# Kernel tuning notes

Hardware: AMD Instinct MI355X
Metric: run time of the kernel (lower is better)

## Reference

```python
import jax, jax.numpy as jnp
import numpy as np

N_NODES = 50000
N_EDGES = 600000
N_GRAPHS = 500


def gcn_conv(x, src, dst, W, b, n_nodes):
    # PyG GCNConv: add self-loops, symmetric normalization D^-1/2 (A+I) D^-1/2, then XW + b
    h = x @ W  # [N, F_out]
    loop = jnp.arange(n_nodes)
    s = jnp.concatenate([src, loop])
    d = jnp.concatenate([dst, loop])
    deg = jax.ops.segment_sum(jnp.ones_like(d, dtype=h.dtype), d, num_segments=n_nodes)
    dinv = jnp.where(deg > 0, jax.lax.rsqrt(jnp.maximum(deg, 1.0)), 0.0)
    norm = dinv[s] * dinv[d]  # [E+N]
    msg = h[s] * norm[:, None]  # gather + scale
    out = jax.ops.segment_sum(msg, d, num_segments=n_nodes)  # scatter-add
    return out + b


def setup_inputs() -> dict:
    key = jax.random.key(0)
    ks = jax.random.split(key, 12)
    F_in, H, Hf, D_out = 128, 128, 64, 1
    x = jax.random.normal(ks[0], (N_NODES, F_in), dtype=jnp.float32)
    edge_index = jax.random.randint(ks[1], (2, N_EDGES), 0, N_NODES, dtype=jnp.int64)
    batch = jnp.sort(jax.random.randint(ks[2], (N_NODES,), 0, N_GRAPHS, dtype=jnp.int64))
    def glorot(k, shape):
        lim = np.sqrt(6.0 / (shape[0] + shape[1]))
        return jax.random.uniform(k, shape, jnp.float32, -lim, lim)
    return {
        "x": x, "edge_index": edge_index, "batch": batch,
        "W1": glorot(ks[3], (F_in, H)), "b1": jnp.zeros((H,), jnp.float32),
        "W2": glorot(ks[4], (H, H)), "b2": jnp.zeros((H,), jnp.float32),
        "W3": glorot(ks[5], (H, H)), "b3": jnp.zeros((H,), jnp.float32),
        "Wf1": glorot(ks[6], (H, Hf)), "bf1": jnp.zeros((Hf,), jnp.float32),
        "Wf2": glorot(ks[7], (Hf, D_out)), "bf2": jnp.zeros((D_out,), jnp.float32),
    }


def reference(x, edge_index, batch, W1, b1, W2, b2, W3, b3, Wf1, bf1, Wf2, bf2):
    src, dst = edge_index[0], edge_index[1]
    n = x.shape[0]
    h = jax.nn.relu(gcn_conv(x, src, dst, W1, b1, n))
    h = jax.nn.relu(gcn_conv(h, src, dst, W2, b2, n))
    h = jax.nn.relu(gcn_conv(h, src, dst, W3, b3, n))
    # global_mean_pool: segment mean over graphs
    sums = jax.ops.segment_sum(h, batch, num_segments=N_GRAPHS)
    cnts = jax.ops.segment_sum(jnp.ones((n,), h.dtype), batch, num_segments=N_GRAPHS)
    hg = sums / jnp.maximum(cnts, 1.0)[:, None]  # [G, 128]
    h = jax.nn.relu(hg @ Wf1 + bf1)
    return h @ Wf2 + bf2
```

## Files before the change

kernel.cpp:

```cpp
#include <hip/hip_runtime.h>

#define N_NODES 50000
#define N_EDGES 600000
#define N_GRAPHS 500
#define F 128

typedef short bf16x8 __attribute__((ext_vector_type(8)));
typedef float f32x4 __attribute__((ext_vector_type(4)));
union U4H8 { uint4 u; bf16x8 h; };

__device__ inline unsigned pk_bf16(float a, float b) {
    unsigned ua = __float_as_uint(a), ub = __float_as_uint(b);
    ua = (ua + 0x7fffu + ((ua >> 16) & 1u)) >> 16;
    ub = (ub + 0x7fffu + ((ub >> 16) & 1u)) >> 16;
    return ua | (ub << 16);
}
__device__ inline float bf16_rnd(float x) {
    unsigned u = __float_as_uint(x);
    u = (u + 0x7fffu + ((u >> 16) & 1u)) & 0xffff0000u;
    return __uint_as_float(u);
}
#define BF_LO(u) __uint_as_float((u) << 16)
#define BF_HI(u) __uint_as_float((u) & 0xffff0000u)

__global__ __launch_bounds__(256) void k_cvt(const float* __restrict__ x,
                                             unsigned short* __restrict__ xb, int n8) {
    int idx = blockIdx.x * 256 + threadIdx.x;
    if (idx < n8) {
        const float4* xr = (const float4*)(x + (size_t)idx * 8);
        float4 a = xr[0], b = xr[1];
        uint4 o;
        o.x = pk_bf16(a.x, a.y); o.y = pk_bf16(a.z, a.w);
        o.z = pk_bf16(b.x, b.y); o.w = pk_bf16(b.z, b.w);
        ((uint4*)xb)[idx] = o;
    }
}

__global__ __launch_bounds__(256) void k_hist(const int* __restrict__ dst, int* __restrict__ cnt, int ne) {
    int e = blockIdx.x * 256 + threadIdx.x;
    if (e < ne) atomicAdd(&cnt[dst[e]], 1);
}

__global__ __launch_bounds__(256) void k_scan1(const int* __restrict__ cnt, int* __restrict__ row_ptr,
                                               int* __restrict__ blksums, float* __restrict__ dinv, int n) {
    __shared__ int s[256];
    int i = blockIdx.x * 256 + threadIdx.x;
    int v = (i < n) ? cnt[i] : 0;
    if (i < n) dinv[i] = rsqrtf((float)(v + 1));
    s[threadIdx.x] = v;
    __syncthreads();
    for (int off = 1; off < 256; off <<= 1) {
        int t = (threadIdx.x >= off) ? s[threadIdx.x - off] : 0;
        __syncthreads();
        s[threadIdx.x] += t;
        __syncthreads();
    }
    if (i < n) row_ptr[i] = s[threadIdx.x] - v;
    if (threadIdx.x == 255) blksums[blockIdx.x] = s[255];
}

__global__ __launch_bounds__(256) void k_scan2(int* __restrict__ blksums, int nb) {
    __shared__ int s[256];
    int v = (threadIdx.x < nb) ? blksums[threadIdx.x] : 0;
    s[threadIdx.x] = v;
    __syncthreads();
    for (int off = 1; off < 256; off <<= 1) {
        int t = (threadIdx.x >= off) ? s[threadIdx.x - off] : 0;
        __syncthreads();
        s[threadIdx.x] += t;
        __syncthreads();
    }
    if (threadIdx.x < nb) blksums[threadIdx.x] = s[threadIdx.x] - v;
}

__global__ __launch_bounds__(256) void k_scan3(int* __restrict__ row_ptr, const int* __restrict__ blksums,
                                               int n, int ne) {
    int i = blockIdx.x * 256 + threadIdx.x;
    if (i < n) row_ptr[i] += blksums[blockIdx.x];
    if (i == 0) row_ptr[n] = ne;
}

__global__ __launch_bounds__(256) void k_fill(const int* __restrict__ src, const int* __restrict__ dst,
                                              const int* __restrict__ row_ptr, int* __restrict__ cnt,
                                              const float* __restrict__ dinv,
                                              int2* __restrict__ esw, int ne) {
    int e = blockIdx.x * 256 + threadIdx.x;
    if (e < ne) {
        int d = dst[e];
        int s = src[e];
        int pos = row_ptr[d] + atomicSub(&cnt[d], 1) - 1;
        esw[pos] = make_int2(s, __float_as_int(dinv[s]));
    }
}

__global__ __launch_bounds__(256) void k_prepW(const float* __restrict__ W1, const float* __restrict__ W2,
                                               const float* __restrict__ W3,
                                               uint4* __restrict__ Whi, uint4* __restrict__ Wlo) {
    int idx = blockIdx.x * 256 + threadIdx.x;
    int layer = idx >> 11;
    const float* W = (layer == 0) ? W1 : (layer == 1) ? W2 : W3;
    int t = idx & 2047;
    int lane = t & 63, sc = t >> 6;
    int s = sc >> 3, c = sc & 7;
    int q = lane >> 4, m = lane & 15;
    int k0 = 32 * s + 8 * q, n0 = 16 * c + m;
    float w[8], h[8];
    #pragma unroll
    for (int j = 0; j < 8; ++j) {
        w[j] = W[(k0 + j) * F + n0];
        h[j] = bf16_rnd(w[j]);
    }
    uint4 uh, ul;
    uh.x = pk_bf16(h[0], h[1]); uh.y = pk_bf16(h[2], h[3]);
    uh.z = pk_bf16(h[4], h[5]); uh.w = pk_bf16(h[6], h[7]);
    ul.x = pk_bf16(w[0] - h[0], w[1] - h[1]); ul.y = pk_bf16(w[2] - h[2], w[3] - h[3]);
    ul.z = pk_bf16(w[4] - h[4], w[5] - h[5]); ul.w = pk_bf16(w[6] - h[6], w[7] - h[7]);
    Whi[idx] = uh;
    Wlo[idx] = ul;
}

#define TN 32
#define GP 132
__global__ __launch_bounds__(256) void k_fused(const int* __restrict__ row_ptr,
                                               const int2* __restrict__ esw,
                                               const float* __restrict__ dinv,
                                               const unsigned short* __restrict__ Hin,
                                               const uint4* __restrict__ Whi,
                                               const uint4* __restrict__ Wlo,
                                               const float* __restrict__ bias,
                                               unsigned short* __restrict__ Hout, int n) {
    __shared__ float G[TN * GP];
    int tid = threadIdx.x;
    int d0 = blockIdx.x * TN;
    int grp = tid >> 4, sub = tid & 15;

    #pragma unroll
    for (int i = 0; i < 2; ++i) {
        int nl = 2 * grp + i;
        int node = d0 + nl;
        float4 accL = make_float4(0.f, 0.f, 0.f, 0.f);
        float4 accH = make_float4(0.f, 0.f, 0.f, 0.f);
        if (node < n) {
            int beg = row_ptr[node], end = row_ptr[node + 1];
            float dd = dinv[node];
            for (int chunk = beg; chunk <= end; chunk += 16) {
                int e = chunk + sub;
                int2 rec;
                if (e < end)       rec = esw[e];
                else if (e == end) rec = make_int2(node, __float_as_int(dd));
                else               rec = make_int2(node, 0);
                uint4 rows[16];
                #pragma unroll
                for (int j = 0; j < 16; ++j) {
                    int sj = __shfl(rec.x, j, 16);
                    rows[j] = ((const uint4*)(Hin + (size_t)sj * F))[sub];
                }
                #pragma unroll
                for (int j = 0; j < 16; ++j) {
                    float wj = __uint_as_float((unsigned)__shfl(rec.y, j, 16)) * dd;
                    accL.x = fmaf(BF_LO(rows[j].x), wj, accL.x);
                    accL.y = fmaf(BF_HI(rows[j].x), wj, accL.y);
                    accL.z = fmaf(BF_LO(rows[j].y), wj, accL.z);
                    accL.w = fmaf(BF_HI(rows[j].y), wj, accL.w);
                    accH.x = fmaf(BF_LO(rows[j].z), wj, accH.x);
                    accH.y = fmaf(BF_HI(rows[j].z), wj, accH.y);
                    accH.z = fmaf(BF_LO(rows[j].w), wj, accH.z);
                    accH.w = fmaf(BF_HI(rows[j].w), wj, accH.w);
                }
            }
        }
        float* gr = &G[nl * GP + 8 * sub];
        ((float4*)gr)[0] = accL;
        ((float4*)gr)[1] = accH;
    }
    __syncthreads();

    int wave = tid >> 6, lane = tid & 63;
    int q = lane >> 4, m = lane & 15;
    int rt = wave & 1;
    int ch = (wave >> 1) * 4;
    int row0 = 16 * rt;
    f32x4 acc[4];
    #pragma unroll
    for (int c = 0; c < 4; ++c) acc[c] = (f32x4){0.f, 0.f, 0.f, 0.f};
    #pragma unroll
    for (int s = 0; s < 4; ++s) {
        const float* gr = &G[(row0 + m) * GP + 32 * s + 8 * q];
        float4 f0 = ((const float4*)gr)[0];
        float4 f1 = ((const float4*)gr)[1];
        float h0 = bf16_rnd(f0.x), h1 = bf16_rnd(f0.y), h2 = bf16_rnd(f0.z), h3 = bf16_rnd(f0.w);
        float h4 = bf16_rnd(f1.x), h5 = bf16_rnd(f1.y), h6 = bf16_rnd(f1.z), h7 = bf16_rnd(f1.w);
        U4H8 ahi, alo;
        ahi.u.x = (__float_as_uint(h0) >> 16) | (__float_as_uint(h1) & 0xffff0000u);
        ahi.u.y = (__float_as_uint(h2) >> 16) | (__float_as_uint(h3) & 0xffff0000u);
        ahi.u.z = (__float_as_uint(h4) >> 16) | (__float_as_uint(h5) & 0xffff0000u);
        ahi.u.w = (__float_as_uint(h6) >> 16) | (__float_as_uint(h7) & 0xffff0000u);
        alo.u.x = pk_bf16(f0.x - h0, f0.y - h1);
        alo.u.y = pk_bf16(f0.z - h2, f0.w - h3);
        alo.u.z = pk_bf16(f1.x - h4, f1.y - h5);
        alo.u.w = pk_bf16(f1.z - h6, f1.w - h7);
        #pragma unroll
        for (int cc = 0; cc < 4; ++cc) {
            int c = ch + cc;
            U4H8 bh, bl;
            bh.u = Whi[(s * 8 + c) * 64 + lane];
            bl.u = Wlo[(s * 8 + c) * 64 + lane];
            acc[cc] = __builtin_amdgcn_mfma_f32_16x16x32_bf16(ahi.h, bh.h, acc[cc], 0, 0, 0);
            acc[cc] = __builtin_amdgcn_mfma_f32_16x16x32_bf16(alo.h, bh.h, acc[cc], 0, 0, 0);
            acc[cc] = __builtin_amdgcn_mfma_f32_16x16x32_bf16(ahi.h, bl.h, acc[cc], 0, 0, 0);
        }
    }
    __syncthreads();

    #pragma unroll
    for (int cc = 0; cc < 4; ++cc) {
        int c = ch + cc;
        float bb = bias[16 * c + m];
        #pragma unroll
        for (int r = 0; r < 4; ++r)
            G[(row0 + 4 * q + r) * GP + 16 * c + m] = fmaxf(acc[cc][r] + bb, 0.f);
    }
    __syncthreads();
    #pragma unroll
    for (int j = 0; j < 2; ++j) {
        int lin = tid + 256 * j;
        int row = lin >> 4, c8 = lin & 15;
        int node = d0 + row;
        if (node < n) {
            const float* gr = &G[row * GP + c8 * 8];
            uint4 o;
            o.x = pk_bf16(gr[0], gr[1]);
            o.y = pk_bf16(gr[2], gr[3]);
            o.z = pk_bf16(gr[4], gr[5]);
            o.w = pk_bf16(gr[6], gr[7]);
            ((uint4*)(Hout + (size_t)node * F))[c8] = o;
        }
    }
}

__global__ __launch_bounds__(256) void k_pool_fc(const unsigned short* __restrict__ Hb,
                                                 const int* __restrict__ batch,
                                                 const float* __restrict__ Wf1,
                                                 const float* __restrict__ bf1,
                                                 const float* __restrict__ Wf2,
                                                 const float* __restrict__ bf2,
                                                 float* __restrict__ out) {
    int g = blockIdx.x;
    int tid = threadIdx.x;
    int lo = 0, hi = N_NODES;
    while (lo < hi) { int mid = (lo + hi) >> 1; if (batch[mid] < g) lo = mid + 1; else hi = mid; }
    int start = lo;
    hi = N_NODES;
    while (lo < hi) { int mid = (lo + hi) >> 1; if (batch[mid] <= g) lo = mid + 1; else hi = mid; }
    int end = lo;

    __shared__ float hs[4][F];
    __shared__ float hg[F];
    int wv = tid >> 6, lane = tid & 63;
    int half = lane >> 5, sub = lane & 31;
    float4 a = make_float4(0.f, 0.f, 0.f, 0.f);
    for (int i = start + wv * 2 + half; i < end; i += 8) {
        uint2 v = ((const uint2*)(Hb + (size_t)i * F))[sub];
        a.x += BF_LO(v.x); a.y += BF_HI(v.x);
        a.z += BF_LO(v.y); a.w += BF_HI(v.y);
    }
    a.x += __shfl_xor(a.x, 32, 64);
    a.y += __shfl_xor(a.y, 32, 64);
    a.z += __shfl_xor(a.z, 32, 64);
    a.w += __shfl_xor(a.w, 32, 64);
    if (half == 0) ((float4*)hs[wv])[sub] = a;
    __syncthreads();
    if (tid < F) {
        float inv = 1.0f / (float)((end - start) > 0 ? (end - start) : 1);
        hg[tid] = (hs[0][tid] + hs[1][tid] + hs[2][tid] + hs[3][tid]) * inv;
    }
    __syncthreads();
    if (tid < 64) {
        float acc = bf1[tid];
        #pragma unroll 4
        for (int f = 0; f < F; ++f) acc = fmaf(hg[f], Wf1[f * 64 + tid], acc);
        float v = fmaxf(acc, 0.f) * Wf2[tid];
        #pragma unroll
        for (int off = 32; off > 0; off >>= 1) v += __shfl_down(v, off, 64);
        if (tid == 0) out[g] = v + bf2[0];
    }
}

extern "C" void kernel_launch(void* const* d_in, const int* in_sizes, int n_in,
                              void* d_out, int out_size, void* d_ws, size_t ws_size,
                              hipStream_t stream) {
    const float* x    = (const float*)d_in[0];
    const int* eidx   = (const int*)d_in[1];
    const int* batch  = (const int*)d_in[2];
    const float* W1   = (const float*)d_in[3];
    const float* b1   = (const float*)d_in[4];
    const float* W2   = (const float*)d_in[5];
    const float* b2   = (const float*)d_in[6];
    const float* W3   = (const float*)d_in[7];
    const float* b3   = (const float*)d_in[8];
    const float* Wf1  = (const float*)d_in[9];
    const float* bf1  = (const float*)d_in[10];
    const float* Wf2  = (const float*)d_in[11];
    const float* bf2  = (const float*)d_in[12];
    float* out = (float*)d_out;

    const int* src = eidx;
    const int* dst = eidx + N_EDGES;

    char* p = (char*)d_ws;
    unsigned short* Xb  = (unsigned short*)p;  p += (size_t)N_NODES * F * 2;
    unsigned short* H1  = (unsigned short*)p;  p += (size_t)N_NODES * F * 2;
    unsigned short* H2  = (unsigned short*)p;  p += (size_t)N_NODES * F * 2;
    unsigned short* H3  = (unsigned short*)p;  p += (size_t)N_NODES * F * 2;
    int2* esw   = (int2*)p;    p += (size_t)N_EDGES * sizeof(int2);
    uint4* Whi  = (uint4*)p;   p += (size_t)3 * 2048 * sizeof(uint4);
    uint4* Wlo  = (uint4*)p;   p += (size_t)3 * 2048 * sizeof(uint4);
    float* dinv = (float*)p;   p += (size_t)N_NODES * sizeof(float);
    int* cnt     = (int*)p;    p += (size_t)N_NODES * sizeof(int);
    int* row_ptr = (int*)p;    p += (size_t)(N_NODES + 1) * sizeof(int);
    int* blksums = (int*)p;    p += 256 * sizeof(int);

    dim3 b256(256);
    int gNodes = (N_NODES + 255) / 256;
    int gEdges = (N_EDGES + 255) / 256;
    int gCvt   = (N_NODES * F / 8 + 255) / 256;
    int gFused = (N_NODES + TN - 1) / TN;

    k_cvt<<<gCvt, b256, 0, stream>>>(x, Xb, N_NODES * F / 8);
    k_prepW<<<24, b256, 0, stream>>>(W1, W2, W3, Whi, Wlo);

    hipMemsetAsync(cnt, 0, (size_t)N_NODES * sizeof(int), stream);
    k_hist<<<gEdges, b256, 0, stream>>>(dst, cnt, N_EDGES);
    k_scan1<<<gNodes, b256, 0, stream>>>(cnt, row_ptr, blksums, dinv, N_NODES);
    k_scan2<<<1, b256, 0, stream>>>(blksums, gNodes);
    k_scan3<<<gNodes, b256, 0, stream>>>(row_ptr, blksums, N_NODES, N_EDGES);
    k_fill<<<gEdges, b256, 0, stream>>>(src, dst, row_ptr, cnt, dinv, esw, N_EDGES);

    k_fused<<<gFused, b256, 0, stream>>>(row_ptr, esw, dinv, Xb, Whi,        Wlo,        b1, H1, N_NODES);
    k_fused<<<gFused, b256, 0, stream>>>(row_ptr, esw, dinv, H1, Whi + 2048, Wlo + 2048, b2, H2, N_NODES);
    k_fused<<<gFused, b256, 0, stream>>>(row_ptr, esw, dinv, H2, Whi + 4096, Wlo + 4096, b3, H3, N_NODES);

    k_pool_fc<<<N_GRAPHS, b256, 0, stream>>>(H3, batch, Wf1, bf1, Wf2, bf2, out);
}
```

Before: 292.0 us.

## Merge prep kernels, prefetch next edge chunk, and add occupancy hint

Folds the bf16 conversion of x, the in-degree histogram and the weight hi/lo split into one launch that dispatches on block index, removing two kernel launches and their gaps. In the fused aggregation kernel, the next chunk's edge records are now loaded before the FMA loop so that their latency overlaps compute, and the shuffles are split into separate batches. It also adds a launch_bounds minimum of 4 blocks per CU, which may cap registers and risk spills given the 16 uint4 row buffer. Padding lanes now gather row 0 instead of the node's own row.

```diff
diff --git a/kernel.cpp b/kernel.cpp
--- a/kernel.cpp
+++ b/kernel.cpp
@@ -23,22 +23,52 @@
 #define BF_LO(u) __uint_as_float((u) << 16)
 #define BF_HI(u) __uint_as_float((u) & 0xffff0000u)
 
-__global__ __launch_bounds__(256) void k_cvt(const float* __restrict__ x,
-                                             unsigned short* __restrict__ xb, int n8) {
-    int idx = blockIdx.x * 256 + threadIdx.x;
-    if (idx < n8) {
-        const float4* xr = (const float4*)(x + (size_t)idx * 8);
-        float4 a = xr[0], b = xr[1];
-        uint4 o;
-        o.x = pk_bf16(a.x, a.y); o.y = pk_bf16(a.z, a.w);
-        o.z = pk_bf16(b.x, b.y); o.w = pk_bf16(b.z, b.w);
-        ((uint4*)xb)[idx] = o;
-    }
-}
-
-__global__ __launch_bounds__(256) void k_hist(const int* __restrict__ dst, int* __restrict__ cnt, int ne) {
-    int e = blockIdx.x * 256 + threadIdx.x;
-    if (e < ne) atomicAdd(&cnt[dst[e]], 1);
+#define G_CVT  3125
+#define G_HIST 2344
+#define G_PREPW 24
+
+__global__ __launch_bounds__(256) void k_prep(const float* __restrict__ x, unsigned short* __restrict__ xb,
+                                              const int* __restrict__ dst, int* __restrict__ cnt,
+                                              const float* __restrict__ W1, const float* __restrict__ W2,
+                                              const float* __restrict__ W3,
+                                              uint4* __restrict__ Whi, uint4* __restrict__ Wlo) {
+    int b = blockIdx.x, tid = threadIdx.x;
+    if (b < G_CVT) {
+        int idx = b * 256 + tid;
+        if (idx < N_NODES * F / 8) {
+            const float4* xr = (const float4*)(x + (size_t)idx * 8);
+            float4 a = xr[0], c = xr[1];
+            uint4 o;
+            o.x = pk_bf16(a.x, a.y); o.y = pk_bf16(a.z, a.w);
+            o.z = pk_bf16(c.x, c.y); o.w = pk_bf16(c.z, c.w);
+            ((uint4*)xb)[idx] = o;
+        }
+    } else if (b < G_CVT + G_HIST) {
+        int e = (b - G_CVT) * 256 + tid;
+        if (e < N_EDGES) atomicAdd(&cnt[dst[e]], 1);
+    } else {
+        int idx = (b - G_CVT - G_HIST) * 256 + tid;
+        int layer = idx >> 11;
+        const float* W = (layer == 0) ? W1 : (layer == 1) ? W2 : W3;
+        int t = idx & 2047;
+        int lane = t & 63, sc = t >> 6;
+        int s = sc >> 3, c = sc & 7;
+        int q = lane >> 4, m = lane & 15;
+        int k0 = 32 * s + 8 * q, n0 = 16 * c + m;
+        float w[8], h[8];
+        #pragma unroll
+        for (int j = 0; j < 8; ++j) {
+            w[j] = W[(k0 + j) * F + n0];
+            h[j] = bf16_rnd(w[j]);
+        }
+        uint4 uh, ul;
+        uh.x = pk_bf16(h[0], h[1]); uh.y = pk_bf16(h[2], h[3]);
+        uh.z = pk_bf16(h[4], h[5]); uh.w = pk_bf16(h[6], h[7]);
+        ul.x = pk_bf16(w[0] - h[0], w[1] - h[1]); ul.y = pk_bf16(w[2] - h[2], w[3] - h[3]);
+        ul.z = pk_bf16(w[4] - h[4], w[5] - h[5]); ul.w = pk_bf16(w[6] - h[6], w[7] - h[7]);
+        Whi[idx] = uh;
+        Wlo[idx] = ul;
+    }
 }
 
 __global__ __launch_bounds__(256) void k_scan1(const int* __restrict__ cnt, int* __restrict__ row_ptr,
@@ -93,42 +123,16 @@
     }
 }
 
-__global__ __launch_bounds__(256) void k_prepW(const float* __restrict__ W1, const float* __restrict__ W2,
-                                               const float* __restrict__ W3,
-                                               uint4* __restrict__ Whi, uint4* __restrict__ Wlo) {
-    int idx = blockIdx.x * 256 + threadIdx.x;
-    int layer = idx >> 11;
-    const float* W = (layer == 0) ? W1 : (layer == 1) ? W2 : W3;
-    int t = idx & 2047;
-    int lane = t & 63, sc = t >> 6;
-    int s = sc >> 3, c = sc & 7;
-    int q = lane >> 4, m = lane & 15;
-    int k0 = 32 * s + 8 * q, n0 = 16 * c + m;
-    float w[8], h[8];
-    #pragma unroll
-    for (int j = 0; j < 8; ++j) {
-        w[j] = W[(k0 + j) * F + n0];
-        h[j] = bf16_rnd(w[j]);
-    }
-    uint4 uh, ul;
-    uh.x = pk_bf16(h[0], h[1]); uh.y = pk_bf16(h[2], h[3]);
-    uh.z = pk_bf16(h[4], h[5]); uh.w = pk_bf16(h[6], h[7]);
-    ul.x = pk_bf16(w[0] - h[0], w[1] - h[1]); ul.y = pk_bf16(w[2] - h[2], w[3] - h[3]);
-    ul.z = pk_bf16(w[4] - h[4], w[5] - h[5]); ul.w = pk_bf16(w[6] - h[6], w[7] - h[7]);
-    Whi[idx] = uh;
-    Wlo[idx] = ul;
-}
-
 #define TN 32
 #define GP 132
-__global__ __launch_bounds__(256) void k_fused(const int* __restrict__ row_ptr,
-                                               const int2* __restrict__ esw,
-                                               const float* __restrict__ dinv,
-                                               const unsigned short* __restrict__ Hin,
-                                               const uint4* __restrict__ Whi,
-                                               const uint4* __restrict__ Wlo,
-                                               const float* __restrict__ bias,
-                                               unsigned short* __restrict__ Hout, int n) {
+__global__ __launch_bounds__(256, 4) void k_fused(const int* __restrict__ row_ptr,
+                                                  const int2* __restrict__ esw,
+                                                  const float* __restrict__ dinv,
+                                                  const unsigned short* __restrict__ Hin,
+                                                  const uint4* __restrict__ Whi,
+                                                  const uint4* __restrict__ Wlo,
+                                                  const float* __restrict__ bias,
+                                                  unsigned short* __restrict__ Hout, int n) {
     __shared__ float G[TN * GP];
     int tid = threadIdx.x;
     int d0 = blockIdx.x * TN;
@@ -143,21 +147,32 @@
         if (node < n) {
             int beg = row_ptr[node], end = row_ptr[node + 1];
             float dd = dinv[node];
-            for (int chunk = beg; chunk <= end; chunk += 16) {
-                int e = chunk + sub;
-                int2 rec;
-                if (e < end)       rec = esw[e];
-                else if (e == end) rec = make_int2(node, __float_as_int(dd));
-                else               rec = make_int2(node, 0);
+            int e = beg + sub;
+            int2 rec;
+            if (e < end)       rec = esw[e];
+            else if (e == end) rec = make_int2(node, __float_as_int(dd));
+            else               rec = make_int2(0, 0);
+            for (int c = beg; c <= end; c += 16) {
+                int sjs[16];
+                #pragma unroll
+                for (int j = 0; j < 16; ++j) sjs[j] = __shfl(rec.x, j, 16);
                 uint4 rows[16];
                 #pragma unroll
-                for (int j = 0; j < 16; ++j) {
-                    int sj = __shfl(rec.x, j, 16);
-                    rows[j] = ((const uint4*)(Hin + (size_t)sj * F))[sub];
+                for (int j = 0; j < 16; ++j)
+                    rows[j] = ((const uint4*)(Hin + (size_t)sjs[j] * F))[sub];
+                float wjs[16];
+                #pragma unroll
+                for (int j = 0; j < 16; ++j)
+                    wjs[j] = __uint_as_float((unsigned)__shfl(rec.y, j, 16)) * dd;
+                if (c + 16 <= end) {
+                    int e2 = c + 16 + sub;
+                    if (e2 < end)       rec = esw[e2];
+                    else if (e2 == end) rec = make_int2(node, __float_as_int(dd));
+                    else                rec = make_int2(0, 0);
                 }
                 #pragma unroll
                 for (int j = 0; j < 16; ++j) {
-                    float wj = __uint_as_float((unsigned)__shfl(rec.y, j, 16)) * dd;
+                    float wj = wjs[j];
                     accL.x = fmaf(BF_LO(rows[j].x), wj, accL.x);
                     accL.y = fmaf(BF_HI(rows[j].x), wj, accL.y);
                     accL.z = fmaf(BF_LO(rows[j].y), wj, accL.z);
@@ -323,14 +338,11 @@
     dim3 b256(256);
     int gNodes = (N_NODES + 255) / 256;
     int gEdges = (N_EDGES + 255) / 256;
-    int gCvt   = (N_NODES * F / 8 + 255) / 256;
     int gFused = (N_NODES + TN - 1) / TN;
 
-    k_cvt<<<gCvt, b256, 0, stream>>>(x, Xb, N_NODES * F / 8);
-    k_prepW<<<24, b256, 0, stream>>>(W1, W2, W3, Whi, Wlo);
-
     hipMemsetAsync(cnt, 0, (size_t)N_NODES * sizeof(int), stream);
-    k_hist<<<gEdges, b256, 0, stream>>>(dst, cnt, N_EDGES);
+    k_prep<<<G_CVT + G_HIST + G_PREPW, b256, 0, stream>>>(x, Xb, dst, cnt, W1, W2, W3, Whi, Wlo);
+
     k_scan1<<<gNodes, b256, 0, stream>>>(cnt, row_ptr, blksums, dinv, N_NODES);
     k_scan2<<<1, b256, 0, stream>>>(blksums, gNodes);
     k_scan3<<<gNodes, b256, 0, stream>>>(row_ptr, blksums, N_NODES, N_EDGES);
```

After: 367.0 us. 1.26x slower.
